# Kernel optimization log

Hardware: AMD Instinct MI355X
Metric: run time of the kernel (lower is better)

Reference implementation:

```python
import jax, jax.numpy as jnp
import numpy as np

N_NODES = 100000


def _gcn_layer(x, W, b, src, dst, n):
    # PyG GCNConv: x' = D^-1/2 (A+I) D^-1/2 (x W) + b, with self-loops added.
    x = x @ W  # [N, out]
    loop = jnp.arange(n, dtype=src.dtype)
    src_f = jnp.concatenate([src, loop])
    dst_f = jnp.concatenate([dst, loop])
    deg = jax.ops.segment_sum(jnp.ones_like(dst_f, dtype=x.dtype), dst_f, num_segments=n)
    dinv = jnp.where(deg > 0, jax.lax.rsqrt(deg), 0.0)
    norm = dinv[src_f] * dinv[dst_f]  # [E+N]
    msgs = x[src_f] * norm[:, None]   # gather + scale
    out = jax.ops.segment_sum(msgs, dst_f, num_segments=n)
    return out + b


def setup_inputs() -> dict:
    key = jax.random.key(0)
    ks = jax.random.split(key, 16)
    inputFeatures = jax.random.normal(ks[0], (N_NODES, 64), dtype=jnp.float32)
    edge_index = jax.random.randint(ks[1], (2, 1000000), 0, N_NODES, dtype=jnp.int64)

    def lin(k, fan_in, fan_out):
        s = 1.0 / np.sqrt(fan_in)
        return jax.random.uniform(k, (fan_in, fan_out), jnp.float32, -s, s)

    return {
        "inputFeatures": inputFeatures,
        "W1": lin(ks[2], 64, 100), "b1": jnp.zeros((100,), jnp.float32),
        "W2": lin(ks[3], 100, 50), "b2": jnp.zeros((50,), jnp.float32),
        "W3": lin(ks[4], 50, 25), "b3": jnp.zeros((25,), jnp.float32),
        "Wl1": lin(ks[5], 25, 25), "bl1": jnp.zeros((25,), jnp.float32),
        "Wl2": lin(ks[6], 25, 10), "bl2": jnp.zeros((10,), jnp.float32),
        "Wl3": lin(ks[7], 10, 1), "bl3": jnp.zeros((1,), jnp.float32),
        "edge_index": edge_index,
    }


def reference(inputFeatures, W1, b1, W2, b2, W3, b3, Wl1, bl1, Wl2, bl2, Wl3, bl3, edge_index):
    src, dst = edge_index[0], edge_index[1]
    n = inputFeatures.shape[0]
    x = jax.nn.relu(_gcn_layer(inputFeatures, W1, b1, src, dst, n))
    x = jax.nn.relu(_gcn_layer(x, W2, b2, src, dst, n))
    x = jax.nn.relu(_gcn_layer(x, W3, b3, src, dst, n))
    x = jax.nn.relu(x @ Wl1 + bl1)
    x = jax.nn.relu(x @ Wl2 + bl2)
    x = jax.nn.relu(x @ Wl3 + bl3)
    return x  # [N, 1]
```

## Files before the change

### kernel.cpp

```cpp
#include <hip/hip_runtime.h>
#include <hip/hip_fp16.h>
#include <cstdint>

constexpr int BSHIFT = 9;
constexpr int NBUCK  = 256;
constexpr int BUCKET_CAP = 6144;

struct alignas(16) H8 { __half2 a, b, c, d; };
struct alignas(8)  H4 { __half2 a, b; };

__device__ __forceinline__ float4 add4(float4 a, float4 b) {
    return make_float4(a.x + b.x, a.y + b.y, a.z + b.z, a.w + b.w);
}
__device__ __forceinline__ float4 mul4s(float4 a, float s) {
    return make_float4(a.x * s, a.y * s, a.z * s, a.w * s);
}
__device__ __forceinline__ void acc_h8(float4& A0, float4& A1, const H8 v, float s) {
    float2 f0 = __half22float2(v.a), f1 = __half22float2(v.b);
    float2 f2 = __half22float2(v.c), f3 = __half22float2(v.d);
    A0.x = fmaf(f0.x, s, A0.x); A0.y = fmaf(f0.y, s, A0.y);
    A0.z = fmaf(f1.x, s, A0.z); A0.w = fmaf(f1.y, s, A0.w);
    A1.x = fmaf(f2.x, s, A1.x); A1.y = fmaf(f2.y, s, A1.y);
    A1.z = fmaf(f3.x, s, A1.z); A1.w = fmaf(f3.y, s, A1.w);
}


constexpr int EPT = 16;
__global__ __launch_bounds__(256) void partition_edges(
    const int* __restrict__ src, const int* __restrict__ dst,
    int* __restrict__ bucketCur, int* __restrict__ pairs, int ne) {
    __shared__ int lcnt[NBUCK];
    __shared__ int lbase[NBUCK];
    int base = blockIdx.x * (256 * EPT);
    if (threadIdx.x < NBUCK) lcnt[threadIdx.x] = 0;
    __syncthreads();
    int2 ed[EPT];
    int  rnk[EPT];
#pragma unroll
    for (int j = 0; j < EPT; ++j) {
        int e = base + j * 256 + threadIdx.x;
        if (e < ne) {
            int d = dst[e];
            ed[j] = make_int2(src[e], d);
            rnk[j] = atomicAdd(&lcnt[d >> BSHIFT], 1);
        } else {
            ed[j].y = -1;
        }
    }
    __syncthreads();
    if (threadIdx.x < NBUCK) {
        int c = lcnt[threadIdx.x];
        lbase[threadIdx.x] = c ? atomicAdd(&bucketCur[threadIdx.x], c) : 0;
    }
    __syncthreads();
#pragma unroll
    for (int j = 0; j < EPT; ++j) {
        if (ed[j].y >= 0) {
            int b = ed[j].y >> BSHIFT;
            int p = lbase[b] + rnk[j];
            if (p < BUCKET_CAP)
                pairs[(size_t)b * BUCKET_CAP + p] =
                    (ed[j].x << BSHIFT) | (ed[j].y & ((1 << BSHIFT) - 1));
        }
    }
}

__global__ void scan_buckets(const int* __restrict__ bucketCnt, int* __restrict__ bucketBase,
                             int* __restrict__ offs, int n, int ne, int nbuckets) {
    __shared__ int tmp[256];
    int c = (threadIdx.x < (unsigned)nbuckets) ? bucketCnt[threadIdx.x] : 0;
    tmp[threadIdx.x] = c;
    __syncthreads();
    for (int off = 1; off < 256; off <<= 1) {
        int t = (threadIdx.x >= (unsigned)off) ? tmp[threadIdx.x - off] : 0;
        __syncthreads();
        tmp[threadIdx.x] += t;
        __syncthreads();
    }
    if (threadIdx.x < (unsigned)nbuckets) bucketBase[threadIdx.x] = tmp[threadIdx.x] - c;
    if (threadIdx.x == 0) offs[n] = ne;
}

__global__ __launch_bounds__(256) void bucket_csr(
    const int* __restrict__ pairs, const int* __restrict__ bucketCnt,
    const int* __restrict__ bucketBase, int* __restrict__ offs,
    float* __restrict__ dinv, int* __restrict__ csr, int n) {
    constexpr int BN = 1 << BSHIFT;
    __shared__ int hist[BN];
    __shared__ int cur[BN];
    __shared__ int tmp[256];
    int b = blockIdx.x;
    int cnt  = bucketCnt[b];
    int base = bucketBase[b];
    const int* pb = pairs + (size_t)b * BUCKET_CAP;
    int nodeLo = b << BSHIFT;

    hist[threadIdx.x] = 0;
    hist[threadIdx.x + 256] = 0;
    __syncthreads();
    for (int e = threadIdx.x; e < cnt; e += 256)
        atomicAdd(&hist[pb[e] & (BN - 1)], 1);
    __syncthreads();

    int l0 = 2 * threadIdx.x, l1 = l0 + 1;
    int h0 = hist[l0], h1 = hist[l1];
    tmp[threadIdx.x] = h0 + h1;
    __syncthreads();
    for (int off = 1; off < 256; off <<= 1) {
        int t = (threadIdx.x >= (unsigned)off) ? tmp[threadIdx.x - off] : 0;
        __syncthreads();
        tmp[threadIdx.x] += t;
        __syncthreads();
    }
    int e0 = tmp[threadIdx.x] - (h0 + h1);
    int e1 = e0 + h0;
    int g0 = nodeLo + l0, g1 = nodeLo + l1;
    if (g0 < n) { offs[g0] = base + e0; dinv[g0] = rsqrtf((float)(h0 + 1)); }
    if (g1 < n) { offs[g1] = base + e1; dinv[g1] = rsqrtf((float)(h1 + 1)); }
    cur[l0] = e0;
    cur[l1] = e1;
    __syncthreads();

    for (int e = threadIdx.x; e < cnt; e += 256) {
        int p = pb[e];
        int pos = atomicAdd(&cur[p & (BN - 1)], 1);
        csr[base + pos] = ((unsigned)p) >> BSHIFT;
    }
}

__global__ void cvt_f32_f16(const float* __restrict__ x, __half* __restrict__ o, int n4) {
    int i = blockIdx.x * blockDim.x + threadIdx.x;
    if (i < n4) {
        float4 v = ((const float4*)x)[i];
        H4 h;
        h.a = __floats2half2_rn(v.x, v.y);
        h.b = __floats2half2_rn(v.z, v.w);
        ((H4*)o)[i] = h;
    }
}

__global__ __launch_bounds__(256) void agg1_h(
    const __half* __restrict__ s, const int* __restrict__ offs,
    const int* __restrict__ csr, const float* __restrict__ dinv,
    __half* __restrict__ out, int n) {
    int lane = threadIdx.x & 7;
    int node = blockIdx.x * 32 + (threadIdx.x >> 3);
    if (node >= n) return;
    int f0 = lane * 8;
    float dv = dinv[node];

    float4 z = make_float4(0.f, 0.f, 0.f, 0.f);
    float4 a00 = z, a01 = z, a10 = z, a11 = z, a20 = z, a21 = z, a30 = z, a31 = z;
    {
        H8 sv = *(const H8*)&s[(size_t)node * 64 + f0];
        acc_h8(a00, a01, sv, dv);
    }
    int e0 = offs[node], e1 = offs[node + 1];
    int e = e0;
    for (; e + 4 <= e1; e += 4) {
        int i0 = csr[e], i1 = csr[e + 1], i2 = csr[e + 2], i3 = csr[e + 3];
        H8 v0 = *(const H8*)&s[(size_t)i0 * 64 + f0];
        H8 v1 = *(const H8*)&s[(size_t)i1 * 64 + f0];
        H8 v2 = *(const H8*)&s[(size_t)i2 * 64 + f0];
        H8 v3 = *(const H8*)&s[(size_t)i3 * 64 + f0];
        acc_h8(a00, a01, v0, dinv[i0]);
        acc_h8(a10, a11, v1, dinv[i1]);
        acc_h8(a20, a21, v2, dinv[i2]);
        acc_h8(a30, a31, v3, dinv[i3]);
    }
    for (; e < e1; ++e) {
        int sid = csr[e];
        H8 v = *(const H8*)&s[(size_t)sid * 64 + f0];
        acc_h8(a00, a01, v, dinv[sid]);
    }
    float4 A0 = add4(add4(a00, a10), add4(a20, a30));
    float4 A1 = add4(add4(a01, a11), add4(a21, a31));
    A0 = mul4s(A0, dv);
    A1 = mul4s(A1, dv);

    H8 h;
    h.a = __floats2half2_rn(A0.x, A0.y);
    h.b = __floats2half2_rn(A0.z, A0.w);
    h.c = __floats2half2_rn(A1.x, A1.y);
    h.d = __floats2half2_rn(A1.z, A1.w);
    *(H8*)&out[(size_t)node * 64 + f0] = h;
}

__global__ __launch_bounds__(256) void agg2_h16(
    const __half* __restrict__ s, const int* __restrict__ offs,
    const int* __restrict__ csr, const float* __restrict__ dinv,
    const float* __restrict__ b, __half* __restrict__ out, int n) {
    constexpr int MH = 50, SH = 64;
    int lane = threadIdx.x & 7;
    int node = blockIdx.x * 32 + (threadIdx.x >> 3);
    if (node >= n) return;
    int f0 = lane * 8;
    H8 zh{};
    if (f0 >= 56) {
        *(H8*)&out[(size_t)node * SH + f0] = zh;
        return;
    }
    float dv = dinv[node];

    float4 z = make_float4(0.f, 0.f, 0.f, 0.f);
    float4 a00 = z, a01 = z, a10 = z, a11 = z, a20 = z, a21 = z, a30 = z, a31 = z;
    {
        H8 sv = *(const H8*)&s[(size_t)node * SH + f0];
        acc_h8(a00, a01, sv, 1.0f);
    }
    int e0 = offs[node], e1 = offs[node + 1];
    int e = e0;
    for (; e + 4 <= e1; e += 4) {
        int i0 = csr[e], i1 = csr[e + 1], i2 = csr[e + 2], i3 = csr[e + 3];
        H8 v0 = *(const H8*)&s[(size_t)i0 * SH + f0];
        H8 v1 = *(const H8*)&s[(size_t)i1 * SH + f0];
        H8 v2 = *(const H8*)&s[(size_t)i2 * SH + f0];
        H8 v3 = *(const H8*)&s[(size_t)i3 * SH + f0];
        acc_h8(a00, a01, v0, 1.0f);
        acc_h8(a10, a11, v1, 1.0f);
        acc_h8(a20, a21, v2, 1.0f);
        acc_h8(a30, a31, v3, 1.0f);
    }
    for (; e < e1; ++e) {
        H8 v = *(const H8*)&s[(size_t)csr[e] * SH + f0];
        acc_h8(a00, a01, v, 1.0f);
    }
    float4 A0 = add4(add4(a00, a10), add4(a20, a30));
    float4 A1 = add4(add4(a01, a11), add4(a21, a31));
    float v[8] = {A0.x, A0.y, A0.z, A0.w, A1.x, A1.y, A1.z, A1.w};
#pragma unroll
    for (int i = 0; i < 8; ++i)
        v[i] = (f0 + i < MH) ? fmaxf(dv * v[i] + b[f0 + i], 0.0f) : 0.0f;
    H8 h;
    h.a = __floats2half2_rn(v[0], v[1]);
    h.b = __floats2half2_rn(v[2], v[3]);
    h.c = __floats2half2_rn(v[4], v[5]);
    h.d = __floats2half2_rn(v[6], v[7]);
    *(H8*)&out[(size_t)node * SH + f0] = h;
}

template <int K, int M, int NT, int XS, int OS, bool SCALE, bool BIAS_RELU, int KR>
__global__ __launch_bounds__(256) void gemm_tiled_h(
    const __half* __restrict__ x, const float* __restrict__ W,
    const float* __restrict__ dinv, const float* __restrict__ b,
    __half* __restrict__ out, int n) {
    static_assert(NT % 4 == 0 && K % 4 == 0 && OS % 4 == 0, "");
    constexpr int Mp  = (M + 3) & ~3;
    constexpr int MQ  = Mp / 4;
    constexpr int NTp = NT + 4;
    constexpr int NTILES = (NT / 4) * MQ;
    static_assert(NTILES <= 256, "");
    static_assert(M % 4 != 0 || KR == K, "float4 W path assumes KR==K");

    __shared__ float Xs[K * NTp];
    __shared__ float Ws[K * Mp];

    if constexpr (M % 4 == 0) {
        for (int i = threadIdx.x; i < K * M / 4; i += 256)
            ((float4*)Ws)[i] = ((const float4*)W)[i];
    } else if constexpr (M % 2 == 0) {
        constexpr int C2 = Mp / 2;
        for (int i = threadIdx.x; i < K * C2; i += 256) {
            int r = i / C2, c = i - r * C2;
            float2 v = make_float2(0.0f, 0.0f);
            if (r < KR) {
                if (c * 2 + 1 < M)  v = *(const float2*)&W[r * M + c * 2];
                else if (c * 2 < M) v = make_float2(W[r * M + c * 2], 0.0f);
            }
            *(float2*)&Ws[r * Mp + c * 2] = v;
        }
    } else {
        for (int i = threadIdx.x; i < K * Mp; i += 256) {
            int r = i / Mp, c = i - r * Mp;
            Ws[i] = (c < M && r < KR) ? W[r * M + c] : 0.0f;
        }
    }

    int nodeBase = blockIdx.x * NT;
    constexpr int KVH = (K % 8 == 0) ? 8 : 4;
    for (int it = threadIdx.x; it < NT * (K / KVH); it += 256) {
        int node = it % NT;
        int kv = it / NT;
        int gn = nodeBase + node;
        if constexpr (KVH == 8) {
            H8 h{};
            if (gn < n) h = *(const H8*)&x[(size_t)gn * XS + kv * 8];
            float2 f0_ = __half22float2(h.a), f1_ = __half22float2(h.b);
            float2 f2_ = __half22float2(h.c), f3_ = __half22float2(h.d);
            Xs[(kv * 8 + 0) * NTp + node] = f0_.x;
            Xs[(kv * 8 + 1) * NTp + node] = f0_.y;
            Xs[(kv * 8 + 2) * NTp + node] = f1_.x;
            Xs[(kv * 8 + 3) * NTp + node] = f1_.y;
            Xs[(kv * 8 + 4) * NTp + node] = f2_.x;
            Xs[(kv * 8 + 5) * NTp + node] = f2_.y;
            Xs[(kv * 8 + 6) * NTp + node] = f3_.x;
            Xs[(kv * 8 + 7) * NTp + node] = f3_.y;
        } else {
            H4 h{};
            if (gn < n) h = *(const H4*)&x[(size_t)gn * XS + kv * 4];
            float2 f0_ = __half22float2(h.a), f1_ = __half22float2(h.b);
            Xs[(kv * 4 + 0) * NTp + node] = f0_.x;
            Xs[(kv * 4 + 1) * NTp + node] = f0_.y;
            Xs[(kv * 4 + 2) * NTp + node] = f1_.x;
            Xs[(kv * 4 + 3) * NTp + node] = f1_.y;
        }
    }
    __syncthreads();

    int t = threadIdx.x;
    if (t >= NTILES) return;
    int ng = t / MQ, mq = t - ng * MQ;
    int n0 = ng * 4;
    int m0 = mq * 4;

    float acc[4][4];
#pragma unroll
    for (int j = 0; j < 4; ++j)
#pragma unroll
        for (int i = 0; i < 4; ++i) acc[j][i] = 0.0f;

#pragma unroll 4
    for (int k = 0; k < K; ++k) {
        float4 xv = *(const float4*)&Xs[k * NTp + n0];
        float4 wv = *(const float4*)&Ws[k * Mp + m0];
        acc[0][0] = fmaf(xv.x, wv.x, acc[0][0]); acc[0][1] = fmaf(xv.x, wv.y, acc[0][1]);
        acc[0][2] = fmaf(xv.x, wv.z, acc[0][2]); acc[0][3] = fmaf(xv.x, wv.w, acc[0][3]);
        acc[1][0] = fmaf(xv.y, wv.x, acc[1][0]); acc[1][1] = fmaf(xv.y, wv.y, acc[1][1]);
        acc[1][2] = fmaf(xv.y, wv.z, acc[1][2]); acc[1][3] = fmaf(xv.y, wv.w, acc[1][3]);
        acc[2][0] = fmaf(xv.z, wv.x, acc[2][0]); acc[2][1] = fmaf(xv.z, wv.y, acc[2][1]);
        acc[2][2] = fmaf(xv.z, wv.z, acc[2][2]); acc[2][3] = fmaf(xv.z, wv.w, acc[2][3]);
        acc[3][0] = fmaf(xv.w, wv.x, acc[3][0]); acc[3][1] = fmaf(xv.w, wv.y, acc[3][1]);
        acc[3][2] = fmaf(xv.w, wv.z, acc[3][2]); acc[3][3] = fmaf(xv.w, wv.w, acc[3][3]);
    }

#pragma unroll
    for (int j = 0; j < 4; ++j) {
        int nd = nodeBase + n0 + j;
        if (nd >= n) continue;
        float dv = SCALE ? dinv[nd] : 1.0f;
        float r[4];
#pragma unroll
        for (int i = 0; i < 4; ++i) {
            r[i] = acc[j][i];
            if (SCALE) r[i] *= dv;
            if (BIAS_RELU) r[i] = fmaxf(r[i] + b[m0 + i], 0.0f);
        }
        if (m0 + 3 < M) {
            H4 h;
            h.a = __floats2half2_rn(r[0], r[1]);
            h.b = __floats2half2_rn(r[2], r[3]);
            *(H4*)&out[(size_t)nd * OS + m0] = h;
        } else {
#pragma unroll
            for (int i = 0; i < 4; ++i)
                if (m0 + i < M) out[(size_t)nd * OS + m0 + i] = __float2half_rn(r[i]);
        }
    }
}

__global__ __launch_bounds__(256) void agg3_mlp_h(
    const __half* __restrict__ s, const int* __restrict__ offs,
    const int* __restrict__ csr, const float* __restrict__ dinv,
    const float* __restrict__ bg,
    const float* __restrict__ Wl1, const float* __restrict__ bl1,
    const float* __restrict__ Wl2, const float* __restrict__ bl2,
    const float* __restrict__ Wl3, const float* __restrict__ bl3,
    float* __restrict__ out, int n) {
    constexpr int MH = 25, SH = 32, LPN = 4;
    __shared__ float W1s[625], W2s[250], W3s[10], b1s[25], b2s[10];
    __shared__ float accs[64 * 26];
    __shared__ float b3s;

    for (int i = threadIdx.x; i < 625; i += 256) W1s[i] = Wl1[i];
    for (int i = threadIdx.x; i < 250; i += 256) W2s[i] = Wl2[i];
    if (threadIdx.x < 10) { W3s[threadIdx.x] = Wl3[threadIdx.x]; b2s[threadIdx.x] = bl2[threadIdx.x]; }
    if (threadIdx.x < 25) b1s[threadIdx.x] = bl1[threadIdx.x];
    if (threadIdx.x == 0) b3s = bl3[0];

    int lane = threadIdx.x % LPN;
    int nl   = threadIdx.x / LPN;
    int node = blockIdx.x * 64 + nl;
    int f0 = lane * 8;

    if (node < n && f0 < MH) {
        float dv = dinv[node];
        float4 z = make_float4(0.f, 0.f, 0.f, 0.f);
        float4 a00 = z, a01 = z, a10 = z, a11 = z, a20 = z, a21 = z, a30 = z, a31 = z;
        {
            H8 sv = *(const H8*)&s[(size_t)node * SH + f0];
            acc_h8(a00, a01, sv, 1.0f);
        }
        int e0 = offs[node], e1 = offs[node + 1];
        int e = e0;
        for (; e + 4 <= e1; e += 4) {
            int i0 = csr[e], i1 = csr[e + 1], i2 = csr[e + 2], i3 = csr[e + 3];
            H8 v0 = *(const H8*)&s[(size_t)i0 * SH + f0];
            H8 v1 = *(const H8*)&s[(size_t)i1 * SH + f0];
            H8 v2 = *(const H8*)&s[(size_t)i2 * SH + f0];
            H8 v3 = *(const H8*)&s[(size_t)i3 * SH + f0];
            acc_h8(a00, a01, v0, 1.0f);
            acc_h8(a10, a11, v1, 1.0f);
            acc_h8(a20, a21, v2, 1.0f);
            acc_h8(a30, a31, v3, 1.0f);
        }
        for (; e < e1; ++e) {
            H8 v = *(const H8*)&s[(size_t)csr[e] * SH + f0];
            acc_h8(a00, a01, v, 1.0f);
        }
        float4 A0 = add4(add4(a00, a10), add4(a20, a30));
        float4 A1 = add4(add4(a01, a11), add4(a21, a31));
        float v[8] = {A0.x, A0.y, A0.z, A0.w, A1.x, A1.y, A1.z, A1.w};
#pragma unroll
        for (int i = 0; i < 8; ++i)
            if (f0 + i < MH)
                accs[nl * 26 + f0 + i] = fmaxf(dv * v[i] + bg[f0 + i], 0.0f);
    }
    __syncthreads();

    if (threadIdx.x < 64) {
        int nd = blockIdx.x * 64 + threadIdx.x;
        if (nd < n) {
            const float* xr = &accs[threadIdx.x * 26];
            float h1[25];
#pragma unroll
            for (int m = 0; m < 25; ++m) {
                float a = b1s[m];
#pragma unroll
                for (int k = 0; k < 25; ++k) a = fmaf(xr[k], W1s[k * 25 + m], a);
                h1[m] = fmaxf(a, 0.0f);
            }
            float h2[10];
#pragma unroll
            for (int m = 0; m < 10; ++m) {
                float a = b2s[m];
#pragma unroll
                for (int k = 0; k < 25; ++k) a = fmaf(h1[k], W2s[k * 10 + m], a);
                h2[m] = fmaxf(a, 0.0f);
            }
            float a = b3s;
#pragma unroll
            for (int k = 0; k < 10; ++k) a = fmaf(h2[k], W3s[k], a);
            out[nd] = fmaxf(a, 0.0f);
        }
    }
}


extern "C" void kernel_launch(void* const* d_in, const int* in_sizes, int n_in,
                              void* d_out, int out_size, void* d_ws, size_t ws_size,
                              hipStream_t stream) {
    const float* x0  = (const float*)d_in[0];
    const float* W1  = (const float*)d_in[1];
    const float* b1  = (const float*)d_in[2];
    const float* W2  = (const float*)d_in[3];
    const float* b2  = (const float*)d_in[4];
    const float* W3  = (const float*)d_in[5];
    const float* b3  = (const float*)d_in[6];
    const float* Wl1 = (const float*)d_in[7];
    const float* bl1 = (const float*)d_in[8];
    const float* Wl2 = (const float*)d_in[9];
    const float* bl2 = (const float*)d_in[10];
    const float* Wl3 = (const float*)d_in[11];
    const float* bl3 = (const float*)d_in[12];
    const int*   edge = (const int*)d_in[13];

    int n  = in_sizes[0] / 64;
    int ne = in_sizes[13] / 2;
    const int* esrc = edge;
    const int* edst = edge + ne;

    char* ws = (char*)d_ws;
    auto alloc = [&](size_t bytes) {
        char* p = ws;
        ws += (bytes + 255) & ~(size_t)255;
        return p;
    };
    int*    offs       = (int*)alloc((size_t)(n + 1) * 4);
    int*    bucketCur  = (int*)alloc(NBUCK * 4);
    int*    bucketBase = (int*)alloc(NBUCK * 4);
    int*    csr        = (int*)alloc((size_t)ne * 4);
    float*  dinv       = (float*)alloc((size_t)n * 4);
    __half* x0h        = (__half*)alloc((size_t)n * 64 * 2);
    __half* bufAh      = (__half*)alloc((size_t)n * 64 * 2);
    __half* bufBh      = (__half*)alloc((size_t)n * 112 * 2);
    __half* bufDh      = (__half*)alloc((size_t)n * 64 * 2);
    int*    pairs = (int*)bufBh;
    __half* bufEh = x0h;
    __half* bufCh = bufAh;
    (void)ws_size; (void)n_in; (void)out_size;

    int nbuckets = (n + (1 << BSHIFT) - 1) >> BSHIFT;

    hipMemsetAsync(bucketCur, 0, NBUCK * 4, stream);
    partition_edges<<<(ne + 256 * EPT - 1) / (256 * EPT), 256, 0, stream>>>(
        esrc, edst, bucketCur, pairs, ne);
    scan_buckets<<<1, 256, 0, stream>>>(bucketCur, bucketBase, offs, n, ne, nbuckets);
    bucket_csr<<<nbuckets, 256, 0, stream>>>(pairs, bucketCur, bucketBase, offs, dinv, csr, n);

    cvt_f32_f16<<<(n * 16 + 255) / 256, 256, 0, stream>>>(x0, x0h, n * 16);

    agg1_h<<<(n + 31) / 32, 256, 0, stream>>>(x0h, offs, csr, dinv, bufAh, n);

    gemm_tiled_h<64, 100, 40, 64, 112, false, true, 64><<<(n + 39) / 40, 256, 0, stream>>>(
        bufAh, W1, nullptr, b1, bufBh, n);

    gemm_tiled_h<100, 50, 64, 112, 64, true, false, 100><<<(n + 63) / 64, 256, 0, stream>>>(
        bufBh, W2, dinv, nullptr, bufDh, n);

    agg2_h16<<<(n + 31) / 32, 256, 0, stream>>>(bufDh, offs, csr, dinv, b2, bufEh, n);

    gemm_tiled_h<52, 25, 144, 64, 32, true, false, 50><<<(n + 143) / 144, 256, 0, stream>>>(
        bufEh, W3, dinv, nullptr, bufCh, n);

    agg3_mlp_h<<<(n + 63) / 64, 256, 0, stream>>>(
        bufCh, offs, csr, dinv, b3, Wl1, bl1, Wl2, bl2, Wl3, bl3, (float*)d_out, n);
}
```

Baseline: 283.8 us.

## Fuse layer-1 and layer-2 GEMMs and pre-scale input by dinv

Merges the two back-to-back GEMMs (64→100 with bias+ReLU, then 100→50 with dinv scaling) into one kernel that keeps the 100-wide hidden tile in shared memory. This removes the write and re-read of the n×112 fp16 intermediate buffer. The first aggregation also no longer gathers dinv per neighbor: the input is pre-scaled by dinv during the fp32→fp16 conversion. The cost is that every block converts both weight matrices to fp16 in shared memory, and the larger shared footprint may lower occupancy. Weights are now fp16 and x is rounded after scaling, which may shift accuracy slightly.

```diff
diff --git a/kernel.cpp b/kernel.cpp
--- a/kernel.cpp
+++ b/kernel.cpp
@@ -128,13 +128,15 @@
     }
 }
 
-__global__ void cvt_f32_f16(const float* __restrict__ x, __half* __restrict__ o, int n4) {
+__global__ void cvt_scale_f32_f16(const float* __restrict__ x, const float* __restrict__ dinv,
+                                  __half* __restrict__ o, int n4) {
     int i = blockIdx.x * blockDim.x + threadIdx.x;
     if (i < n4) {
+        float dv = dinv[i >> 4];
         float4 v = ((const float4*)x)[i];
         H4 h;
-        h.a = __floats2half2_rn(v.x, v.y);
-        h.b = __floats2half2_rn(v.z, v.w);
+        h.a = __floats2half2_rn(v.x * dv, v.y * dv);
+        h.b = __floats2half2_rn(v.z * dv, v.w * dv);
         ((H4*)o)[i] = h;
     }
 }
@@ -153,7 +155,7 @@
     float4 a00 = z, a01 = z, a10 = z, a11 = z, a20 = z, a21 = z, a30 = z, a31 = z;
     {
         H8 sv = *(const H8*)&s[(size_t)node * 64 + f0];
-        acc_h8(a00, a01, sv, dv);
+        acc_h8(a00, a01, sv, 1.0f);
     }
     int e0 = offs[node], e1 = offs[node + 1];
     int e = e0;
@@ -163,15 +165,15 @@
         H8 v1 = *(const H8*)&s[(size_t)i1 * 64 + f0];
         H8 v2 = *(const H8*)&s[(size_t)i2 * 64 + f0];
         H8 v3 = *(const H8*)&s[(size_t)i3 * 64 + f0];
-        acc_h8(a00, a01, v0, dinv[i0]);
-        acc_h8(a10, a11, v1, dinv[i1]);
-        acc_h8(a20, a21, v2, dinv[i2]);
-        acc_h8(a30, a31, v3, dinv[i3]);
+        acc_h8(a00, a01, v0, 1.0f);
+        acc_h8(a10, a11, v1, 1.0f);
+        acc_h8(a20, a21, v2, 1.0f);
+        acc_h8(a30, a31, v3, 1.0f);
     }
     for (; e < e1; ++e) {
         int sid = csr[e];
         H8 v = *(const H8*)&s[(size_t)sid * 64 + f0];
-        acc_h8(a00, a01, v, dinv[sid]);
+        acc_h8(a00, a01, v, 1.0f);
     }
     float4 A0 = add4(add4(a00, a10), add4(a20, a30));
     float4 A1 = add4(add4(a01, a11), add4(a21, a31));
@@ -237,6 +239,124 @@
     h.c = __floats2half2_rn(v[4], v[5]);
     h.d = __floats2half2_rn(v[6], v[7]);
     *(H8*)&out[(size_t)node * SH + f0] = h;
+}
+
+constexpr int G12_NT = 40;
+__global__ __launch_bounds__(256) void gemm12_fused(
+    const __half* __restrict__ x, const float* __restrict__ W1, const float* __restrict__ b1,
+    const float* __restrict__ W2, const float* __restrict__ dinv,
+    __half* __restrict__ out, int n) {
+    constexpr int K1 = 64, M1 = 100, M2 = 50, M2p = 52, XS = 64, OS = 64;
+    constexpr int NT = G12_NT, NTp = NT + 4;
+
+    __shared__ float  Xs[K1 * NTp];
+    __shared__ float  Hs[M1 * NTp];
+    __shared__ __half W1h[K1 * M1];
+    __shared__ __half W2h[M1 * M2p];
+    __shared__ float  b1s[M1];
+
+    for (int i = threadIdx.x; i < K1 * M1 / 4; i += 256) {
+        float4 v = ((const float4*)W1)[i];
+        H4 h;
+        h.a = __floats2half2_rn(v.x, v.y);
+        h.b = __floats2half2_rn(v.z, v.w);
+        ((H4*)W1h)[i] = h;
+    }
+    {
+        constexpr int C2 = M2p / 2;
+        for (int i = threadIdx.x; i < M1 * C2; i += 256) {
+            int r = i / C2, c = i - r * C2;
+            float2 v = make_float2(0.0f, 0.0f);
+            if (c * 2 + 1 < M2) v = *(const float2*)&W2[r * M2 + c * 2];
+            *(__half2*)&W2h[r * M2p + c * 2] = __floats2half2_rn(v.x, v.y);
+        }
+    }
+    for (int i = threadIdx.x; i < M1; i += 256) b1s[i] = b1[i];
+
+    int nodeBase = blockIdx.x * NT;
+    for (int it = threadIdx.x; it < NT * (K1 / 8); it += 256) {
+        int node = it % NT;
+        int kv = it / NT;
+        int gn = nodeBase + node;
+        H8 h{};
+        if (gn < n) h = *(const H8*)&x[(size_t)gn * XS + kv * 8];
+        float2 f0_ = __half22float2(h.a), f1_ = __half22float2(h.b);
+        float2 f2_ = __half22float2(h.c), f3_ = __half22float2(h.d);
+        Xs[(kv * 8 + 0) * NTp + node] = f0_.x;
+        Xs[(kv * 8 + 1) * NTp + node] = f0_.y;
+        Xs[(kv * 8 + 2) * NTp + node] = f1_.x;
+        Xs[(kv * 8 + 3) * NTp + node] = f1_.y;
+        Xs[(kv * 8 + 4) * NTp + node] = f2_.x;
+        Xs[(kv * 8 + 5) * NTp + node] = f2_.y;
+        Xs[(kv * 8 + 6) * NTp + node] = f3_.x;
+        Xs[(kv * 8 + 7) * NTp + node] = f3_.y;
+    }
+    __syncthreads();
+
+    {
+        constexpr int MQ1 = M1 / 4;
+        int t = threadIdx.x;
+        if (t < (NT / 4) * MQ1) {
+            int ng = t / MQ1, mq = t - ng * MQ1;
+            int n0 = ng * 4, m0 = mq * 4;
+            float acc[4][4] = {};
+#pragma unroll 4
+            for (int k = 0; k < K1; ++k) {
+                float4 xv = *(const float4*)&Xs[k * NTp + n0];
+                H4 wh = *(const H4*)&W1h[k * M1 + m0];
+                float2 w01 = __half22float2(wh.a), w23 = __half22float2(wh.b);
+                acc[0][0] = fmaf(xv.x, w01.x, acc[0][0]); acc[0][1] = fmaf(xv.x, w01.y, acc[0][1]);
+                acc[0][2] = fmaf(xv.x, w23.x, acc[0][2]); acc[0][3] = fmaf(xv.x, w23.y, acc[0][3]);
+                acc[1][0] = fmaf(xv.y, w01.x, acc[1][0]); acc[1][1] = fmaf(xv.y, w01.y, acc[1][1]);
+                acc[1][2] = fmaf(xv.y, w23.x, acc[1][2]); acc[1][3] = fmaf(xv.y, w23.y, acc[1][3]);
+                acc[2][0] = fmaf(xv.z, w01.x, acc[2][0]); acc[2][1] = fmaf(xv.z, w01.y, acc[2][1]);
+                acc[2][2] = fmaf(xv.z, w23.x, acc[2][2]); acc[2][3] = fmaf(xv.z, w23.y, acc[2][3]);
+                acc[3][0] = fmaf(xv.w, w01.x, acc[3][0]); acc[3][1] = fmaf(xv.w, w01.y, acc[3][1]);
+                acc[3][2] = fmaf(xv.w, w23.x, acc[3][2]); acc[3][3] = fmaf(xv.w, w23.y, acc[3][3]);
+            }
+#pragma unroll
+            for (int i = 0; i < 4; ++i) {
+                float bb = b1s[m0 + i];
+#pragma unroll
+                for (int j = 0; j < 4; ++j)
+                    Hs[(m0 + i) * NTp + (n0 + j)] = fmaxf(acc[j][i] + bb, 0.0f);
+            }
+        }
+    }
+    __syncthreads();
+
+    {
+        constexpr int MQ2 = M2p / 4;
+        int t = threadIdx.x;
+        if (t >= (NT / 4) * MQ2) return;
+        int ng = t / MQ2, mq = t - ng * MQ2;
+        int n0 = ng * 4, m0 = mq * 4;
+        float acc[4][4] = {};
+#pragma unroll 4
+        for (int k = 0; k < M1; ++k) {
+            float4 xv = *(const float4*)&Hs[k * NTp + n0];
+            H4 wh = *(const H4*)&W2h[k * M2p + m0];
+            float2 w01 = __half22float2(wh.a), w23 = __half22float2(wh.b);
+            acc[0][0] = fmaf(xv.x, w01.x, acc[0][0]); acc[0][1] = fmaf(xv.x, w01.y, acc[0][1]);
+            acc[0][2] = fmaf(xv.x, w23.x, acc[0][2]); acc[0][3] = fmaf(xv.x, w23.y, acc[0][3]);
+            acc[1][0] = fmaf(xv.y, w01.x, acc[1][0]); acc[1][1] = fmaf(xv.y, w01.y, acc[1][1]);
+            acc[1][2] = fmaf(xv.y, w23.x, acc[1][2]); acc[1][3] = fmaf(xv.y, w23.y, acc[1][3]);
+            acc[2][0] = fmaf(xv.z, w01.x, acc[2][0]); acc[2][1] = fmaf(xv.z, w01.y, acc[2][1]);
+            acc[2][2] = fmaf(xv.z, w23.x, acc[2][2]); acc[2][3] = fmaf(xv.z, w23.y, acc[2][3]);
+            acc[3][0] = fmaf(xv.w, w01.x, acc[3][0]); acc[3][1] = fmaf(xv.w, w01.y, acc[3][1]);
+            acc[3][2] = fmaf(xv.w, w23.x, acc[3][2]); acc[3][3] = fmaf(xv.w, w23.y, acc[3][3]);
+        }
+#pragma unroll
+        for (int j = 0; j < 4; ++j) {
+            int nd = nodeBase + n0 + j;
+            if (nd >= n) continue;
+            float dv = dinv[nd];
+            H4 h;
+            h.a = __floats2half2_rn(acc[j][0] * dv, acc[j][1] * dv);
+            h.b = __floats2half2_rn(acc[j][2] * dv, acc[j][3] * dv);
+            *(H4*)&out[(size_t)nd * OS + m0] = h;
+        }
+    }
 }
 
 template <int K, int M, int NT, int XS, int OS, bool SCALE, bool BIAS_RELU, int KR>
@@ -482,9 +602,8 @@
     float*  dinv       = (float*)alloc((size_t)n * 4);
     __half* x0h        = (__half*)alloc((size_t)n * 64 * 2);
     __half* bufAh      = (__half*)alloc((size_t)n * 64 * 2);
-    __half* bufBh      = (__half*)alloc((size_t)n * 112 * 2);
     __half* bufDh      = (__half*)alloc((size_t)n * 64 * 2);
-    int*    pairs = (int*)bufBh;
+    int*    pairs = (int*)bufDh;
     __half* bufEh = x0h;
     __half* bufCh = bufAh;
     (void)ws_size; (void)n_in; (void)out_size;
@@ -497,15 +616,12 @@
     scan_buckets<<<1, 256, 0, stream>>>(bucketCur, bucketBase, offs, n, ne, nbuckets);
     bucket_csr<<<nbuckets, 256, 0, stream>>>(pairs, bucketCur, bucketBase, offs, dinv, csr, n);
 
-    cvt_f32_f16<<<(n * 16 + 255) / 256, 256, 0, stream>>>(x0, x0h, n * 16);
+    cvt_scale_f32_f16<<<(n * 16 + 255) / 256, 256, 0, stream>>>(x0, dinv, x0h, n * 16);
 
     agg1_h<<<(n + 31) / 32, 256, 0, stream>>>(x0h, offs, csr, dinv, bufAh, n);
 
-    gemm_tiled_h<64, 100, 40, 64, 112, false, true, 64><<<(n + 39) / 40, 256, 0, stream>>>(
-        bufAh, W1, nullptr, b1, bufBh, n);
-
-    gemm_tiled_h<100, 50, 64, 112, 64, true, false, 100><<<(n + 63) / 64, 256, 0, stream>>>(
-        bufBh, W2, dinv, nullptr, bufDh, n);
+    gemm12_fused<<<(n + G12_NT - 1) / G12_NT, 256, 0, stream>>>(
+        bufAh, W1, b1, W2, dinv, bufDh, n);
 
     agg2_h16<<<(n + 31) / 32, 256, 0, stream>>>(bufDh, offs, csr, dinv, b2, bufEh, n);
 
```

After: 285.0 us. No clear change (+0.4%).

## Replace scalar GEMMs with fused MFMA kernels and prescale inputs by dinv

Applied to the files above, without the earlier changes.

Replaces the three FP32-FMA shared-memory GEMMs with MFMA f16 kernels that use weights pre-packed into the MFMA fragment layout. Layers 1 and 2 are fused into one kernel, and the 100-wide hidden activation stays in LDS instead of going through a global buffer. The dinv source scaling for layer 1 moves into the input conversion kernel, which removes the per-edge dinv gathers in agg1. In exchange it adds a small weight-packing launch, and the W1 and W2 weights are now rounded to f16, so precision drops slightly.

```diff
diff --git a/kernel.cpp b/kernel.cpp
--- a/kernel.cpp
+++ b/kernel.cpp
@@ -8,6 +8,9 @@
 
 struct alignas(16) H8 { __half2 a, b, c, d; };
 struct alignas(8)  H4 { __half2 a, b; };
+
+typedef _Float16 f16x8 __attribute__((ext_vector_type(8)));
+typedef float    f32x4 __attribute__((ext_vector_type(4)));
 
 __device__ __forceinline__ float4 add4(float4 a, float4 b) {
     return make_float4(a.x + b.x, a.y + b.y, a.z + b.z, a.w + b.w);
@@ -128,13 +131,43 @@
     }
 }
 
-__global__ void cvt_f32_f16(const float* __restrict__ x, __half* __restrict__ o, int n4) {
+__global__ void pack_weights(const float* __restrict__ W1, const float* __restrict__ W2,
+                             const float* __restrict__ W3,
+                             __half* __restrict__ P1, __half* __restrict__ P2,
+                             __half* __restrict__ P3) {
+    int t = threadIdx.x;
+    for (int i = t; i < 7 * 2 * 64 * 8; i += 256) {
+        int j = i & 7, lane = (i >> 3) & 63, f = i >> 9;
+        int mt = f >> 1, kf = f & 1;
+        int k = kf * 32 + (lane >> 4) * 8 + j;
+        int m = mt * 16 + (lane & 15);
+        P1[i] = __float2half_rn(m < 100 ? W1[k * 100 + m] : 0.0f);
+    }
+    for (int i = t; i < 4 * 4 * 64 * 8; i += 256) {
+        int j = i & 7, lane = (i >> 3) & 63, f = i >> 9;
+        int mt = f >> 2, kf = f & 3;
+        int k = kf * 32 + (lane >> 4) * 8 + j;
+        int m = mt * 16 + (lane & 15);
+        P2[i] = __float2half_rn((k < 100 && m < 50) ? W2[k * 50 + m] : 0.0f);
+    }
+    for (int i = t; i < 2 * 2 * 64 * 8; i += 256) {
+        int j = i & 7, lane = (i >> 3) & 63, f = i >> 9;
+        int mt = f >> 1, kf = f & 1;
+        int k = kf * 32 + (lane >> 4) * 8 + j;
+        int m = mt * 16 + (lane & 15);
+        P3[i] = __float2half_rn((k < 50 && m < 25) ? W3[k * 25 + m] : 0.0f);
+    }
+}
+
+__global__ void cvt_scale_f32_f16(const float* __restrict__ x, const float* __restrict__ dinv,
+                                  __half* __restrict__ o, int n4) {
     int i = blockIdx.x * blockDim.x + threadIdx.x;
     if (i < n4) {
+        float dv = dinv[i >> 4];
         float4 v = ((const float4*)x)[i];
         H4 h;
-        h.a = __floats2half2_rn(v.x, v.y);
-        h.b = __floats2half2_rn(v.z, v.w);
+        h.a = __floats2half2_rn(v.x * dv, v.y * dv);
+        h.b = __floats2half2_rn(v.z * dv, v.w * dv);
         ((H4*)o)[i] = h;
     }
 }
@@ -153,7 +186,7 @@
     float4 a00 = z, a01 = z, a10 = z, a11 = z, a20 = z, a21 = z, a30 = z, a31 = z;
     {
         H8 sv = *(const H8*)&s[(size_t)node * 64 + f0];
-        acc_h8(a00, a01, sv, dv);
+        acc_h8(a00, a01, sv, 1.0f);
     }
     int e0 = offs[node], e1 = offs[node + 1];
     int e = e0;
@@ -163,15 +196,15 @@
         H8 v1 = *(const H8*)&s[(size_t)i1 * 64 + f0];
         H8 v2 = *(const H8*)&s[(size_t)i2 * 64 + f0];
         H8 v3 = *(const H8*)&s[(size_t)i3 * 64 + f0];
-        acc_h8(a00, a01, v0, dinv[i0]);
-        acc_h8(a10, a11, v1, dinv[i1]);
-        acc_h8(a20, a21, v2, dinv[i2]);
-        acc_h8(a30, a31, v3, dinv[i3]);
+        acc_h8(a00, a01, v0, 1.0f);
+        acc_h8(a10, a11, v1, 1.0f);
+        acc_h8(a20, a21, v2, 1.0f);
+        acc_h8(a30, a31, v3, 1.0f);
     }
     for (; e < e1; ++e) {
         int sid = csr[e];
         H8 v = *(const H8*)&s[(size_t)sid * 64 + f0];
-        acc_h8(a00, a01, v, dinv[sid]);
+        acc_h8(a00, a01, v, 1.0f);
     }
     float4 A0 = add4(add4(a00, a10), add4(a20, a30));
     float4 A1 = add4(add4(a01, a11), add4(a21, a31));
@@ -239,121 +272,119 @@
     *(H8*)&out[(size_t)node * SH + f0] = h;
 }
 
-template <int K, int M, int NT, int XS, int OS, bool SCALE, bool BIAS_RELU, int KR>
-__global__ __launch_bounds__(256) void gemm_tiled_h(
-    const __half* __restrict__ x, const float* __restrict__ W,
-    const float* __restrict__ dinv, const float* __restrict__ b,
-    __half* __restrict__ out, int n) {
-    static_assert(NT % 4 == 0 && K % 4 == 0 && OS % 4 == 0, "");
-    constexpr int Mp  = (M + 3) & ~3;
-    constexpr int MQ  = Mp / 4;
-    constexpr int NTp = NT + 4;
-    constexpr int NTILES = (NT / 4) * MQ;
-    static_assert(NTILES <= 256, "");
-    static_assert(M % 4 != 0 || KR == K, "float4 W path assumes KR==K");
-
-    __shared__ float Xs[K * NTp];
-    __shared__ float Ws[K * Mp];
-
-    if constexpr (M % 4 == 0) {
-        for (int i = threadIdx.x; i < K * M / 4; i += 256)
-            ((float4*)Ws)[i] = ((const float4*)W)[i];
-    } else if constexpr (M % 2 == 0) {
-        constexpr int C2 = Mp / 2;
-        for (int i = threadIdx.x; i < K * C2; i += 256) {
-            int r = i / C2, c = i - r * C2;
-            float2 v = make_float2(0.0f, 0.0f);
-            if (r < KR) {
-                if (c * 2 + 1 < M)  v = *(const float2*)&W[r * M + c * 2];
-                else if (c * 2 < M) v = make_float2(W[r * M + c * 2], 0.0f);
+constexpr int HP = 136;
+__global__ __launch_bounds__(256, 4) void gemm12_mfma(
+    const __half* __restrict__ x, const __half* __restrict__ P1,
+    const float* __restrict__ b1, const __half* __restrict__ P2,
+    const float* __restrict__ dinv, __half* __restrict__ out, int n) {
+    __shared__ _Float16 Hs[128 * HP];
+    int tid = threadIdx.x;
+    int lane = tid & 63;
+    int w = tid >> 6;
+    int lg = lane >> 4;
+    int lr = lane & 15;
+    int blockBase = blockIdx.x * 128;
+    int waveBase  = blockBase + w * 32;
+
+    for (int i = tid; i < 128 * 2; i += 256) {
+        f16x8 zz = {};
+        *(f16x8*)&Hs[(i >> 1) * HP + 112 + (i & 1) * 8] = zz;
+    }
+
+    float b1v[7];
+#pragma unroll
+    for (int mt = 0; mt < 7; ++mt) {
+        int m = mt * 16 + lr;
+        b1v[mt] = (m < 100) ? b1[m] : 0.0f;
+    }
+
+    const f16x8* P1v = (const f16x8*)P1;
+#pragma unroll
+    for (int rt = 0; rt < 2; ++rt) {
+        int rowG = waveBase + rt * 16 + lr;
+        f16x8 a0 = {}, a1 = {};
+        if (rowG < n) {
+            a0 = *(const f16x8*)&x[(size_t)rowG * 64 + lg * 8];
+            a1 = *(const f16x8*)&x[(size_t)rowG * 64 + 32 + lg * 8];
+        }
+        int hbase = w * 32 + rt * 16;
+#pragma unroll
+        for (int mt = 0; mt < 7; ++mt) {
+            f16x8 w0 = P1v[(mt * 2 + 0) * 64 + lane];
+            f16x8 w1 = P1v[(mt * 2 + 1) * 64 + lane];
+            f32x4 acc = {};
+            acc = __builtin_amdgcn_mfma_f32_16x16x32_f16(a0, w0, acc, 0, 0, 0);
+            acc = __builtin_amdgcn_mfma_f32_16x16x32_f16(a1, w1, acc, 0, 0, 0);
+            int col = mt * 16 + lr;
+#pragma unroll
+            for (int i = 0; i < 4; ++i) {
+                int rloc = hbase + lg * 4 + i;
+                Hs[rloc * HP + col] = (_Float16)fmaxf(acc[i] + b1v[mt], 0.0f);
             }
-            *(float2*)&Ws[r * Mp + c * 2] = v;
-        }
-    } else {
-        for (int i = threadIdx.x; i < K * Mp; i += 256) {
-            int r = i / Mp, c = i - r * Mp;
-            Ws[i] = (c < M && r < KR) ? W[r * M + c] : 0.0f;
-        }
-    }
-
-    int nodeBase = blockIdx.x * NT;
-    constexpr int KVH = (K % 8 == 0) ? 8 : 4;
-    for (int it = threadIdx.x; it < NT * (K / KVH); it += 256) {
-        int node = it % NT;
-        int kv = it / NT;
-        int gn = nodeBase + node;
-        if constexpr (KVH == 8) {
-            H8 h{};
-            if (gn < n) h = *(const H8*)&x[(size_t)gn * XS + kv * 8];
-            float2 f0_ = __half22float2(h.a), f1_ = __half22float2(h.b);
-            float2 f2_ = __half22float2(h.c), f3_ = __half22float2(h.d);
-            Xs[(kv * 8 + 0) * NTp + node] = f0_.x;
-            Xs[(kv * 8 + 1) * NTp + node] = f0_.y;
-            Xs[(kv * 8 + 2) * NTp + node] = f1_.x;
-            Xs[(kv * 8 + 3) * NTp + node] = f1_.y;
-            Xs[(kv * 8 + 4) * NTp + node] = f2_.x;
-            Xs[(kv * 8 + 5) * NTp + node] = f2_.y;
-            Xs[(kv * 8 + 6) * NTp + node] = f3_.x;
-            Xs[(kv * 8 + 7) * NTp + node] = f3_.y;
-        } else {
-            H4 h{};
-            if (gn < n) h = *(const H4*)&x[(size_t)gn * XS + kv * 4];
-            float2 f0_ = __half22float2(h.a), f1_ = __half22float2(h.b);
-            Xs[(kv * 4 + 0) * NTp + node] = f0_.x;
-            Xs[(kv * 4 + 1) * NTp + node] = f0_.y;
-            Xs[(kv * 4 + 2) * NTp + node] = f1_.x;
-            Xs[(kv * 4 + 3) * NTp + node] = f1_.y;
-        }
-    }
-    __syncthreads();
-
-    int t = threadIdx.x;
-    if (t >= NTILES) return;
-    int ng = t / MQ, mq = t - ng * MQ;
-    int n0 = ng * 4;
-    int m0 = mq * 4;
-
-    float acc[4][4];
-#pragma unroll
-    for (int j = 0; j < 4; ++j)
-#pragma unroll
-        for (int i = 0; i < 4; ++i) acc[j][i] = 0.0f;
-
-#pragma unroll 4
-    for (int k = 0; k < K; ++k) {
-        float4 xv = *(const float4*)&Xs[k * NTp + n0];
-        float4 wv = *(const float4*)&Ws[k * Mp + m0];
-        acc[0][0] = fmaf(xv.x, wv.x, acc[0][0]); acc[0][1] = fmaf(xv.x, wv.y, acc[0][1]);
-        acc[0][2] = fmaf(xv.x, wv.z, acc[0][2]); acc[0][3] = fmaf(xv.x, wv.w, acc[0][3]);
-        acc[1][0] = fmaf(xv.y, wv.x, acc[1][0]); acc[1][1] = fmaf(xv.y, wv.y, acc[1][1]);
-        acc[1][2] = fmaf(xv.y, wv.z, acc[1][2]); acc[1][3] = fmaf(xv.y, wv.w, acc[1][3]);
-        acc[2][0] = fmaf(xv.z, wv.x, acc[2][0]); acc[2][1] = fmaf(xv.z, wv.y, acc[2][1]);
-        acc[2][2] = fmaf(xv.z, wv.z, acc[2][2]); acc[2][3] = fmaf(xv.z, wv.w, acc[2][3]);
-        acc[3][0] = fmaf(xv.w, wv.x, acc[3][0]); acc[3][1] = fmaf(xv.w, wv.y, acc[3][1]);
-        acc[3][2] = fmaf(xv.w, wv.z, acc[3][2]); acc[3][3] = fmaf(xv.w, wv.w, acc[3][3]);
-    }
-
-#pragma unroll
-    for (int j = 0; j < 4; ++j) {
-        int nd = nodeBase + n0 + j;
-        if (nd >= n) continue;
-        float dv = SCALE ? dinv[nd] : 1.0f;
-        float r[4];
-#pragma unroll
-        for (int i = 0; i < 4; ++i) {
-            r[i] = acc[j][i];
-            if (SCALE) r[i] *= dv;
-            if (BIAS_RELU) r[i] = fmaxf(r[i] + b[m0 + i], 0.0f);
-        }
-        if (m0 + 3 < M) {
-            H4 h;
-            h.a = __floats2half2_rn(r[0], r[1]);
-            h.b = __floats2half2_rn(r[2], r[3]);
-            *(H4*)&out[(size_t)nd * OS + m0] = h;
-        } else {
-#pragma unroll
-            for (int i = 0; i < 4; ++i)
-                if (m0 + i < M) out[(size_t)nd * OS + m0 + i] = __float2half_rn(r[i]);
+        }
+    }
+    __syncthreads();
+
+    const f16x8* P2v = (const f16x8*)P2;
+#pragma unroll
+    for (int mt = 0; mt < 4; ++mt) {
+        f16x8 w0 = P2v[(mt * 4 + 0) * 64 + lane];
+        f16x8 w1 = P2v[(mt * 4 + 1) * 64 + lane];
+        f16x8 w2 = P2v[(mt * 4 + 2) * 64 + lane];
+        f16x8 w3 = P2v[(mt * 4 + 3) * 64 + lane];
+#pragma unroll
+        for (int rt = 0; rt < 2; ++rt) {
+            int lbase = w * 32 + rt * 16;
+            const _Float16* hrow = &Hs[(size_t)(lbase + lr) * HP];
+            f16x8 a0 = *(const f16x8*)&hrow[lg * 8];
+            f16x8 a1 = *(const f16x8*)&hrow[32 + lg * 8];
+            f16x8 a2 = *(const f16x8*)&hrow[64 + lg * 8];
+            f16x8 a3 = *(const f16x8*)&hrow[96 + lg * 8];
+            f32x4 acc = {};
+            acc = __builtin_amdgcn_mfma_f32_16x16x32_f16(a0, w0, acc, 0, 0, 0);
+            acc = __builtin_amdgcn_mfma_f32_16x16x32_f16(a1, w1, acc, 0, 0, 0);
+            acc = __builtin_amdgcn_mfma_f32_16x16x32_f16(a2, w2, acc, 0, 0, 0);
+            acc = __builtin_amdgcn_mfma_f32_16x16x32_f16(a3, w3, acc, 0, 0, 0);
+            int col = mt * 16 + lr;
+#pragma unroll
+            for (int i = 0; i < 4; ++i) {
+                int node = blockBase + lbase + lg * 4 + i;
+                if (node < n)
+                    out[(size_t)node * 64 + col] = __float2half_rn(acc[i] * dinv[node]);
+            }
+        }
+    }
+}
+
+__global__ __launch_bounds__(256, 4) void gemm3_mfma(
+    const __half* __restrict__ x, const __half* __restrict__ P3,
+    const float* __restrict__ dinv, __half* __restrict__ out, int n) {
+    int tid = threadIdx.x, lane = tid & 63, w = tid >> 6;
+    int lg = lane >> 4, lr = lane & 15;
+    int waveBase = blockIdx.x * 128 + w * 32;
+    const f16x8* P3v = (const f16x8*)P3;
+    f16x8 w00 = P3v[0 * 64 + lane], w01 = P3v[1 * 64 + lane];
+    f16x8 w10 = P3v[2 * 64 + lane], w11 = P3v[3 * 64 + lane];
+#pragma unroll
+    for (int rt = 0; rt < 2; ++rt) {
+        int rowG = waveBase + rt * 16 + lr;
+        f16x8 a0 = {}, a1 = {};
+        if (rowG < n) {
+            a0 = *(const f16x8*)&x[(size_t)rowG * 64 + lg * 8];
+            a1 = *(const f16x8*)&x[(size_t)rowG * 64 + 32 + lg * 8];
+        }
+#pragma unroll
+        for (int mt = 0; mt < 2; ++mt) {
+            f32x4 acc = {};
+            acc = __builtin_amdgcn_mfma_f32_16x16x32_f16(a0, mt ? w10 : w00, acc, 0, 0, 0);
+            acc = __builtin_amdgcn_mfma_f32_16x16x32_f16(a1, mt ? w11 : w01, acc, 0, 0, 0);
+            int col = mt * 16 + lr;
+#pragma unroll
+            for (int i = 0; i < 4; ++i) {
+                int node = waveBase + rt * 16 + lg * 4 + i;
+                if (node < n)
+                    out[(size_t)node * 32 + col] = __float2half_rn(acc[i] * dinv[node]);
+            }
         }
     }
 }
@@ -482,14 +513,18 @@
     float*  dinv       = (float*)alloc((size_t)n * 4);
     __half* x0h        = (__half*)alloc((size_t)n * 64 * 2);
     __half* bufAh      = (__half*)alloc((size_t)n * 64 * 2);
-    __half* bufBh      = (__half*)alloc((size_t)n * 112 * 2);
     __half* bufDh      = (__half*)alloc((size_t)n * 64 * 2);
-    int*    pairs = (int*)bufBh;
+    __half* P1         = (__half*)alloc(7 * 2 * 64 * 8 * 2);
+    __half* P2         = (__half*)alloc(4 * 4 * 64 * 8 * 2);
+    __half* P3         = (__half*)alloc(2 * 2 * 64 * 8 * 2);
+    int*    pairs = (int*)bufDh;
     __half* bufEh = x0h;
     __half* bufCh = bufAh;
     (void)ws_size; (void)n_in; (void)out_size;
 
     int nbuckets = (n + (1 << BSHIFT) - 1) >> BSHIFT;
+
+    pack_weights<<<1, 256, 0, stream>>>(W1, W2, W3, P1, P2, P3);
 
     hipMemsetAsync(bucketCur, 0, NBUCK * 4, stream);
     partition_edges<<<(ne + 256 * EPT - 1) / (256 * EPT), 256, 0, stream>>>(
@@ -497,20 +532,15 @@
     scan_buckets<<<1, 256, 0, stream>>>(bucketCur, bucketBase, offs, n, ne, nbuckets);
     bucket_csr<<<nbuckets, 256, 0, stream>>>(pairs, bucketCur, bucketBase, offs, dinv, csr, n);
 
-    cvt_f32_f16<<<(n * 16 + 255) / 256, 256, 0, stream>>>(x0, x0h, n * 16);
+    cvt_scale_f32_f16<<<(n * 16 + 255) / 256, 256, 0, stream>>>(x0, dinv, x0h, n * 16);
 
     agg1_h<<<(n + 31) / 32, 256, 0, stream>>>(x0h, offs, csr, dinv, bufAh, n);
 
-    gemm_tiled_h<64, 100, 40, 64, 112, false, true, 64><<<(n + 39) / 40, 256, 0, stream>>>(
-        bufAh, W1, nullptr, b1, bufBh, n);
-
-    gemm_tiled_h<100, 50, 64, 112, 64, true, false, 100><<<(n + 63) / 64, 256, 0, stream>>>(
-        bufBh, W2, dinv, nullptr, bufDh, n);
+    gemm12_mfma<<<(n + 127) / 128, 256, 0, stream>>>(bufAh, P1, b1, P2, dinv, bufDh, n);
 
     agg2_h16<<<(n + 31) / 32, 256, 0, stream>>>(bufDh, offs, csr, dinv, b2, bufEh, n);
 
-    gemm_tiled_h<52, 25, 144, 64, 32, true, false, 50><<<(n + 143) / 144, 256, 0, stream>>>(
-        bufEh, W3, dinv, nullptr, bufCh, n);
+    gemm3_mfma<<<(n + 127) / 128, 256, 0, stream>>>(bufEh, P3, dinv, bufCh, n);
 
     agg3_mlp_h<<<(n + 63) / 64, 256, 0, stream>>>(
         bufCh, offs, csr, dinv, b3, Wl1, bl1, Wl2, bl2, Wl3, bl3, (float*)d_out, n);
```

Result: faster. 253.3 us (-10.7%).
